# Kernel tuning notes

Hardware: AMD Instinct MI355X
Metric: run time of the kernel (lower is better)

Reference implementation:

```python
import jax, jax.numpy as jnp
import numpy as np

# graph/batch constants
B, N_PER, DEG, FEAT, K = 64, 1024, 16, 64, 10
N = B * N_PER            # 65536 total nodes
E = N * DEG              # 1048576 edges
HID = 2 * FEAT           # 128


def setup_inputs() -> dict:
    key = jax.random.key(0)
    ks = jax.random.split(key, 10)
    x = jax.random.normal(ks[0], (N, FEAT), jnp.float32)
    # intra-graph edges: local indices in [0, n) offset by graph id * n
    offs = (jnp.arange(B, dtype=jnp.int32) * N_PER)[:, None]
    edge_src = (jax.random.randint(ks[1], (B, N_PER * DEG), 0, N_PER, jnp.int32) + offs).reshape(-1)
    edge_dst = (jax.random.randint(ks[2], (B, N_PER * DEG), 0, N_PER, jnp.int32) + offs).reshape(-1)
    uniforms = jax.random.uniform(ks[3], (N, 3 * K), jnp.float32, 1e-6, 1.0 - 1e-6)

    def lin(k, i, o):
        s = 1.0 / np.sqrt(i)
        return jax.random.uniform(k, (i, o), jnp.float32, -s, s)

    return {
        "x": x, "edge_src": edge_src, "edge_dst": edge_dst, "uniforms": uniforms,
        "W0": lin(ks[4], FEAT, HID), "b0": jnp.zeros((HID,), jnp.float32),
        "W1": lin(ks[5], HID, HID), "b1": jnp.zeros((HID,), jnp.float32),
        "Wf": lin(ks[6], HID, HID), "bf": jnp.zeros((HID,), jnp.float32),
        "W2": lin(ks[7], 2 * HID, HID), "b2": jnp.zeros((HID,), jnp.float32),
        "W3": lin(ks[8], HID, 1), "b3": jnp.zeros((1,), jnp.float32),
    }


def _gcn_norm(src, dst):
    # GCNConv: add self-loops, symmetric deg^{-1/2} normalization
    loop = jnp.arange(N, dtype=src.dtype)
    s = jnp.concatenate([src, loop])
    d = jnp.concatenate([dst, loop])
    deg = jnp.zeros((N,), jnp.float32).at[d].add(1.0)
    dinv = jax.lax.rsqrt(deg)  # deg >= 1 because of self-loops
    return s, d, dinv[s] * dinv[d]


def _gcn(h, W, b, s, d, norm):
    h = h @ W                                                   # [N, out]
    agg = jnp.zeros((N, W.shape[1]), h.dtype).at[d].add(h[s] * norm[:, None])
    return agg + b


def reference(x, edge_src, edge_dst, uniforms, W0, b0, W1, b1, Wf, bf, W2, b2, W3, b3):
    s, d, norm = _gcn_norm(edge_src, edge_dst)
    # conv0 + global max pool + fc1 -> per-graph global info
    h0 = jax.nn.relu(_gcn(x, W0, b0, s, d, norm))               # [N, HID]
    glob = jnp.max(h0.reshape(B, N_PER, HID), axis=1) @ Wf + bf  # [B, HID]
    # two applications of the SAME conv1 (as in the source)
    h = jax.nn.relu(_gcn(h0, W1, b1, s, d, norm))
    h = jax.nn.relu(_gcn(h, W1, b1, s, d, norm))
    # ConcatenateLayer: [local, tiled global] per node (dropout is eval identity)
    h = jnp.concatenate([h, jnp.repeat(glob, N_PER, axis=0)], axis=-1)  # [N, 2*HID]
    h = jax.nn.relu(_gcn(h, W2, b2, s, d, norm))
    logits = _gcn(h, W3, b3, s, d, norm).reshape(B, N_PER)      # [B, n]
    # SampleConcrete (eval): per-graph top-k threshold mask
    th = jax.lax.top_k(logits, K)[0][:, -1]                     # kth-largest per graph
    mask = (logits >= th[:, None]).astype(jnp.float32)
    return mask.reshape(N, 1)
```

## Files before the change

### kernel.cpp

```cpp
#include <hip/hip_runtime.h>
#include <math.h>

#define NB    64
#define NPER  1024
#define NTOT  65536
#define ETOT  1048576
#define FEAT  64
#define HID   128
#define KSEL  10
#define MAXDEG 64


typedef __attribute__((ext_vector_type(8))) short bf16x8;
typedef __attribute__((ext_vector_type(4))) float f32x4;

static __device__ __forceinline__ unsigned short f2bf(float x) {
    unsigned u = __float_as_uint(x);
    return (unsigned short)((u + 0x7FFFu + ((u >> 16) & 1u)) >> 16);
}
static __device__ __forceinline__ float bf2f(unsigned short s) {
    return __uint_as_float(((unsigned)s) << 16);
}

__global__ __launch_bounds__(256) void csr_k(const int* __restrict__ src,
                                             const int* __restrict__ dst,
                                             int* __restrict__ cnt,
                                             unsigned short* __restrict__ col16) {
    int e = blockIdx.x * 256 + threadIdx.x;
    if (e >= ETOT) return;
    int d = dst[e];
    int s = src[e];
    int pos = atomicAdd(&cnt[d], 1);
    col16[(size_t)pos * NTOT + d] = (unsigned short)(s & (NPER - 1));
}

__global__ __launch_bounds__(256) void pack_k(const float* __restrict__ W0,
                                              const float* __restrict__ W1,
                                              const float* __restrict__ W2,
                                              unsigned short* __restrict__ Wph,
                                              unsigned short* __restrict__ Wpl,
                                              float* __restrict__ part,
                                              int* __restrict__ cnt) {
    int t = blockIdx.x * 256 + threadIdx.x;
    for (int i = t; i < NTOT; i += 160 * 256) cnt[i] = 0;
    if (blockIdx.x == 0) {
        for (int i = threadIdx.x; i < NB * 128; i += 256) part[i] = 0.f;
    }
    if (t >= 320 * 128) return;
    int k = t >> 7;
    int c = t & 127;
    float v;
    size_t mb;
    int kk;
    if (k < 64)       { kk = k;       v = W0[kk * 128 + c]; mb = 0; }
    else if (k < 192) { kk = k - 64;  v = W1[kk * 128 + c]; mb = (size_t)64 * 128; }
    else              { kk = k - 192; v = W2[kk * 128 + c]; mb = (size_t)192 * 128; }
    unsigned short h  = f2bf(v);
    unsigned short lo = f2bf(v - bf2f(h));
    size_t d = mb + ((size_t)(kk >> 3) * 128 + c) * 8 + (kk & 7);
    Wph[d] = h;
    Wpl[d] = lo;
}

__global__ __launch_bounds__(1024) void agg_k(const float* __restrict__ Z,
                                              const float* __restrict__ x,
                                              const unsigned short* __restrict__ col16,
                                              const int* __restrict__ cnt,
                                              unsigned short* __restrict__ Ah,
                                              unsigned short* __restrict__ Al,
                                              int cshift,
                                              float* __restrict__ fvec,
                                              const float* __restrict__ Wf,
                                              const float* __restrict__ bfv,
                                              const float* __restrict__ W2g,
                                              float* __restrict__ gproj,
                                              const float* __restrict__ part) {
    __shared__ float4 sy4[4096];
    int t = threadIdx.x;

    if (Wf && (int)blockIdx.x >= (int)gridDim.x - NB) {
        float* sm = (float*)sy4;
        float* mp = sm;
        float* ps = sm + 128;
        float* gl = sm + 128 + 1024;
        int gg = blockIdx.x - (gridDim.x - NB);
        int o = t & 127, s8 = t >> 7;
        if (t < 128) mp[t] = part[(size_t)gg * 128 + t];
        __syncthreads();
        float p = 0.f;
#pragma unroll
        for (int q = 0; q < 16; ++q) { int k = s8 * 16 + q; p += mp[k] * Wf[(size_t)k * 128 + o]; }
        ps[t] = p;
        __syncthreads();
        if (t < 128) {
            float a = bfv[t];
#pragma unroll
            for (int q = 0; q < 8; ++q) a += ps[q * 128 + t];
            gl[t] = a;
        }
        __syncthreads();
        p = 0.f;
#pragma unroll
        for (int q = 0; q < 16; ++q) { int k = s8 * 16 + q; p += gl[k] * W2g[(size_t)(128 + k) * 128 + o]; }
        ps[t] = p;
        __syncthreads();
        if (t < 128) {
            float a = 0.f;
#pragma unroll
            for (int q = 0; q < 8; ++q) a += ps[q * 128 + t];
            gproj[(size_t)gg * 128 + t] = a;
        }
        return;
    }

    int g = blockIdx.x >> cshift;
    int c = blockIdx.x & ((1 << cshift) - 1);
    int gbase = g << 10;

    if (x) {
#pragma unroll
        for (int j = 0; j < 4; ++j) {
            int fl = j * 1024 + t;
            int v = fl >> 2, q = fl & 3;
            float dvv = rsqrtf((float)cnt[gbase + v] + 1.0f);
            float4 z = *(const float4*)&x[(size_t)(gbase + v) * FEAT + c * 16 + q * 4];
            z.x *= dvv; z.y *= dvv; z.z *= dvv; z.w *= dvv;
            sy4[fl] = z;
        }
    } else {
        const float4* Zg4 = (const float4*)(Z + ((size_t)c * NTOT + gbase) * 16);
#pragma unroll
        for (int j = 0; j < 4; ++j) sy4[j * 1024 + t] = Zg4[j * 1024 + t];
    }
    __syncthreads();

    int f4 = t & 3;
    int vl = t >> 2;

#pragma unroll 1
    for (int pass = 0; pass < 4; ++pass) {
        int v = pass * 256 + vl;
        int gv = gbase + v;
        int n = cnt[gv];
        float dv = rsqrtf((float)n + 1.0f);
        const unsigned short* ip = col16 + gv;
        float4 acc = sy4[v * 4 + f4];
        int i = 0;
        for (; i + 4 <= n; i += 4) {
            int a0 = ip[(size_t)(i + 0) * NTOT];
            int a1 = ip[(size_t)(i + 1) * NTOT];
            int a2 = ip[(size_t)(i + 2) * NTOT];
            int a3 = ip[(size_t)(i + 3) * NTOT];
            float4 y0 = sy4[a0 * 4 + f4];
            float4 y1 = sy4[a1 * 4 + f4];
            float4 y2 = sy4[a2 * 4 + f4];
            float4 y3 = sy4[a3 * 4 + f4];
            acc.x += (y0.x + y1.x) + (y2.x + y3.x);
            acc.y += (y0.y + y1.y) + (y2.y + y3.y);
            acc.z += (y0.z + y1.z) + (y2.z + y3.z);
            acc.w += (y0.w + y1.w) + (y2.w + y3.w);
        }
        for (; i < n; ++i) {
            float4 ya = sy4[(int)ip[(size_t)i * NTOT] * 4 + f4];
            acc.x += ya.x; acc.y += ya.y; acc.z += ya.z; acc.w += ya.w;
        }
        acc.x *= dv; acc.y *= dv; acc.z *= dv; acc.w *= dv;
        int krow = c * 16 + f4 * 4;
        size_t ba = ((size_t)(krow >> 3) * NTOT + gv) * 8 + (krow & 7);
        ushort4 h, lo;
        h.x = f2bf(acc.x); lo.x = f2bf(acc.x - bf2f(h.x));
        h.y = f2bf(acc.y); lo.y = f2bf(acc.y - bf2f(h.y));
        h.z = f2bf(acc.z); lo.z = f2bf(acc.z - bf2f(h.z));
        h.w = f2bf(acc.w); lo.w = f2bf(acc.w - bf2f(h.w));
        *(ushort4*)&Ah[ba] = h;
        *(ushort4*)&Al[ba] = lo;
    }

    if (fvec && c == 0) {
        __syncthreads();
        float* sdv = (float*)sy4;
        float dv = rsqrtf((float)cnt[gbase + t] + 1.0f);
        sdv[t] = dv;
        __syncthreads();
        int n = cnt[gbase + t];
        float acc = dv;
        const unsigned short* ip = col16 + gbase + t;
        for (int i = 0; i < n; ++i) acc += sdv[ip[(size_t)i * NTOT]];
        fvec[gbase + t] = dv * acc;
    }
}

__global__ __launch_bounds__(256, 4) void gemm_k(const unsigned short* __restrict__ Ah,
                                                 const unsigned short* __restrict__ Al,
                                                 const unsigned short* __restrict__ Wph,
                                                 const unsigned short* __restrict__ Wpl,
                                                 const float* __restrict__ bias,
                                                 float* __restrict__ outZ,
                                                 int K,
                                                 const float* __restrict__ fvec,
                                                 const float* __restrict__ gproj,
                                                 float* __restrict__ part,
                                                 const float* __restrict__ W3,
                                                 const int* __restrict__ cnt,
                                                 float* __restrict__ zout) {
    __shared__ __align__(16) unsigned short sAh[64 * 128];
    __shared__ __align__(16) unsigned short sAl[64 * 128];
    __shared__ float zred[4 * 64];

    int t = threadIdx.x;
    int row0 = blockIdx.x * 64;
    int w = t >> 6;
    int l = t & 63;
    int lr = l & 15;
    int hg = l >> 4;

    f32x4 acc[4][2];
#pragma unroll
    for (int m = 0; m < 4; ++m)
#pragma unroll
        for (int n = 0; n < 2; ++n) acc[m][n] = (f32x4){0.f, 0.f, 0.f, 0.f};

    int nu = (K >> 3) << 6 >> 8;
    for (int i = 0; i < nu; ++i) {
        int u = t + i * 256;
        int p = u >> 6, r = u & 63;
        size_t src = ((size_t)p * NTOT + row0 + r) * 8;
        *(uint4*)&sAh[u * 8] = *(const uint4*)&Ah[src];
        *(uint4*)&sAl[u * 8] = *(const uint4*)&Al[src];
    }
    __syncthreads();

    int nk = K >> 5;
#pragma unroll 1
    for (int s = 0; s < nk; ++s) {
        int pb = s * 4 + hg;
        bf16x8 ah[4], al[4], bh[2], bl[2];
#pragma unroll
        for (int m = 0; m < 4; ++m) {
            ah[m] = *(const bf16x8*)&sAh[(pb * 64 + m * 16 + lr) * 8];
            al[m] = *(const bf16x8*)&sAl[(pb * 64 + m * 16 + lr) * 8];
        }
#pragma unroll
        for (int n = 0; n < 2; ++n) {
            size_t wb = ((size_t)pb * 128 + w * 32 + n * 16 + lr) * 8;
            bh[n] = *(const bf16x8*)&Wph[wb];
            bl[n] = *(const bf16x8*)&Wpl[wb];
        }
#pragma unroll
        for (int m = 0; m < 4; ++m)
#pragma unroll
            for (int n = 0; n < 2; ++n) {
                acc[m][n] = __builtin_amdgcn_mfma_f32_16x16x32_bf16(ah[m], bh[n], acc[m][n], 0, 0, 0);
                acc[m][n] = __builtin_amdgcn_mfma_f32_16x16x32_bf16(al[m], bh[n], acc[m][n], 0, 0, 0);
                acc[m][n] = __builtin_amdgcn_mfma_f32_16x16x32_bf16(ah[m], bl[n], acc[m][n], 0, 0, 0);
            }
    }

    int g = row0 >> 10;
    int wc0 = w * 32;
    float bb[2], gp[2], w3c[2];
#pragma unroll
    for (int n = 0; n < 2; ++n) {
        int col = wc0 + n * 16 + lr;
        bb[n]  = bias[col];
        gp[n]  = fvec ? gproj[(size_t)g * 128 + col] : 0.f;
        w3c[n] = zout ? W3[col] : 0.f;
    }
    float fr[4][4];
    if (fvec) {
#pragma unroll
        for (int m = 0; m < 4; ++m)
#pragma unroll
            for (int r = 0; r < 4; ++r) fr[m][r] = fvec[row0 + m * 16 + hg * 4 + r];
    }
    float dvs[4][4];
    if (outZ) {
#pragma unroll
        for (int m = 0; m < 4; ++m)
#pragma unroll
            for (int r = 0; r < 4; ++r)
                dvs[m][r] = rsqrtf((float)cnt[row0 + m * 16 + hg * 4 + r] + 1.0f);
    }
    float zp[4][4];
#pragma unroll
    for (int m = 0; m < 4; ++m)
#pragma unroll
        for (int r = 0; r < 4; ++r) zp[m][r] = 0.f;
    float cmx[2] = {0.f, 0.f};

#pragma unroll
    for (int m = 0; m < 4; ++m)
#pragma unroll
        for (int n = 0; n < 2; ++n)
#pragma unroll
            for (int r = 0; r < 4; ++r) {
                float v = acc[m][n][r] + bb[n];
                if (fvec) v += fr[m][r] * gp[n];
                v = fmaxf(v, 0.f);
                if (part) cmx[n] = fmaxf(cmx[n], v);
                if (zout) zp[m][r] += v * w3c[n];
                if (outZ) {
                    int row = row0 + m * 16 + hg * 4 + r;
                    int cidx = w * 2 + n;
                    outZ[((size_t)cidx * NTOT + row) * 16 + lr] = v * dvs[m][r];
                }
            }

    if (part) {
#pragma unroll
        for (int n = 0; n < 2; ++n) {
            float v = cmx[n];
            v = fmaxf(v, __shfl_xor(v, 16));
            v = fmaxf(v, __shfl_xor(v, 32));
            if (hg == 0)
                atomicMax((int*)&part[(size_t)g * 128 + wc0 + n * 16 + lr],
                          __float_as_int(v));
        }
    }

    if (zout) {
#pragma unroll
        for (int m = 0; m < 4; ++m)
#pragma unroll
            for (int r = 0; r < 4; ++r) {
                float v = zp[m][r];
                v += __shfl_xor(v, 1);
                v += __shfl_xor(v, 2);
                v += __shfl_xor(v, 4);
                v += __shfl_xor(v, 8);
                zp[m][r] = v;
            }
        if (lr == 0) {
#pragma unroll
            for (int m = 0; m < 4; ++m)
#pragma unroll
                for (int r = 0; r < 4; ++r)
                    zred[w * 64 + m * 16 + hg * 4 + r] = zp[m][r];
        }
        __syncthreads();
        if (t < 64) {
            float sZ = zred[t] + zred[64 + t] + zred[128 + t] + zred[192 + t];
            zout[row0 + t] = sZ * rsqrtf((float)cnt[row0 + t] + 1.0f);
        }
    }
}

__global__ __launch_bounds__(1024) void smask_k(const float* __restrict__ z,
                                                const unsigned short* __restrict__ col16,
                                                const int* __restrict__ cnt,
                                                const float* __restrict__ b3,
                                                float* __restrict__ out) {
    __shared__ float sz[1024];
    __shared__ float sl[1024];
    __shared__ float slo[1024];
    __shared__ float rv[16];
    __shared__ int   ri[16];
    __shared__ float sth;
    int g = blockIdx.x, t = threadIdx.x;
    int wv = t >> 6, ln = t & 63;
    int base = g << 10;
    sz[t] = z[base + t];
    __syncthreads();
    float bb = b3[0];
    {
        int gv = base + t;
        int n = cnt[gv];
        float dv = rsqrtf((float)n + 1.0f);
        float acc = sz[t];
        const unsigned short* ip = col16 + gv;
        int j = 0;
        for (; j + 2 <= n; j += 2)
            acc += sz[ip[(size_t)j * NTOT]] + sz[ip[(size_t)(j + 1) * NTOT]];
        for (; j < n; ++j) acc += sz[ip[(size_t)j * NTOT]];
        float lg = acc * dv + bb;
        sl[t] = lg; slo[t] = lg;
    }
    __syncthreads();
    for (int pass = 0; pass < KSEL; ++pass) {
        float bv = sl[t];
        int bi = t;
#pragma unroll
        for (int off = 32; off; off >>= 1) {
            float ov = __shfl_xor(bv, off);
            int   oi = __shfl_xor(bi, off);
            if (ov > bv || (ov == bv && oi < bi)) { bv = ov; bi = oi; }
        }
        if (ln == 0) { rv[wv] = bv; ri[wv] = bi; }
        __syncthreads();
        if (t == 0) {
            float mv = rv[0]; int mi = ri[0];
#pragma unroll
            for (int q = 1; q < 16; ++q)
                if (rv[q] > mv || (rv[q] == mv && ri[q] < mi)) { mv = rv[q]; mi = ri[q]; }
            sth = mv; sl[mi] = -INFINITY;
        }
        __syncthreads();
    }
    float th = sth;
    out[base + t] = (slo[t] >= th) ? 1.f : 0.f;
}

extern "C" void kernel_launch(void* const* d_in, const int* in_sizes, int n_in,
                              void* d_out, int out_size, void* d_ws, size_t ws_size,
                              hipStream_t stream) {
    const float* x        = (const float*)d_in[0];
    const int*   edge_src = (const int*)d_in[1];
    const int*   edge_dst = (const int*)d_in[2];
    const float* W0 = (const float*)d_in[4];
    const float* b0 = (const float*)d_in[5];
    const float* W1 = (const float*)d_in[6];
    const float* b1 = (const float*)d_in[7];
    const float* Wf = (const float*)d_in[8];
    const float* bf = (const float*)d_in[9];
    const float* W2 = (const float*)d_in[10];
    const float* b2 = (const float*)d_in[11];
    const float* W3 = (const float*)d_in[12];
    const float* b3 = (const float*)d_in[13];
    float* out = (float*)d_out;

    char* w = (char*)d_ws;
    int*            cnt   = (int*)w;            w += (size_t)NTOT * 4;
    unsigned short* col16 = (unsigned short*)w; w += (size_t)NTOT * MAXDEG * 2;
    float*          fvec  = (float*)w;          w += (size_t)NTOT * 4;
    unsigned short* Ah    = (unsigned short*)w; w += (size_t)NTOT * 128 * 2;
    unsigned short* Al    = (unsigned short*)w; w += (size_t)NTOT * 128 * 2;
    float*          Q     = (float*)w;          w += (size_t)NTOT * 128 * 4;
    float*          part  = (float*)w;          w += (size_t)NB * 128 * 4;
    float*          gproj = (float*)w;          w += (size_t)NB * 128 * 4;
    float*          z     = (float*)w;          w += (size_t)NTOT * 4;
    unsigned short* Wph   = (unsigned short*)w; w += (size_t)320 * 128 * 2;
    unsigned short* Wpl   = (unsigned short*)w; w += (size_t)320 * 128 * 2;

    pack_k<<<160, 256, 0, stream>>>(W0, W1, W2, Wph, Wpl, part, cnt);
    csr_k<<<ETOT / 256, 256, 0, stream>>>(edge_src, edge_dst, cnt, col16);

    agg_k<<<NB * 4, 1024, 0, stream>>>(nullptr, x, col16, cnt, Ah, Al, 2, nullptr,
                                       nullptr, nullptr, nullptr, nullptr, nullptr);
    gemm_k<<<NTOT / 64, 256, 0, stream>>>(Ah, Al, Wph, Wpl, b0, Q, FEAT,
                                          nullptr, nullptr, part, nullptr, cnt, nullptr);

    agg_k<<<NB * 8 + NB, 1024, 0, stream>>>(Q, nullptr, col16, cnt, Ah, Al, 3, nullptr,
                                            Wf, bf, W2, gproj, part);
    gemm_k<<<NTOT / 64, 256, 0, stream>>>(Ah, Al, Wph + 64 * 128, Wpl + 64 * 128, b1, Q,
                                          HID, nullptr, nullptr, nullptr, nullptr, cnt,
                                          nullptr);
    agg_k<<<NB * 8, 1024, 0, stream>>>(Q, nullptr, col16, cnt, Ah, Al, 3, nullptr,
                                       nullptr, nullptr, nullptr, nullptr, nullptr);
    gemm_k<<<NTOT / 64, 256, 0, stream>>>(Ah, Al, Wph + 64 * 128, Wpl + 64 * 128, b1, Q,
                                          HID, nullptr, nullptr, nullptr, nullptr, cnt,
                                          nullptr);

    agg_k<<<NB * 8, 1024, 0, stream>>>(Q, nullptr, col16, cnt, Ah, Al, 3, fvec,
                                       nullptr, nullptr, nullptr, nullptr, nullptr);
    gemm_k<<<NTOT / 64, 256, 0, stream>>>(Ah, Al, Wph + 192 * 128, Wpl + 192 * 128, b2,
                                          nullptr, HID, fvec, gproj, nullptr, W3, cnt, z);

    smask_k<<<NB, 1024, 0, stream>>>(z, col16, cnt, b3, out);
}
```

Measured before the change: 308.9 us.

## Fuse CSR build and weight packing into one kernel with shared-memory degree counters

Replaces the separate weight-packing and CSR-building kernels with one launch. One block per graph counts incoming edges with shared-memory atomics and writes the local neighbor lists, and extra blocks pack the weights and zero the partial buffer. This removes a kernel launch, the global counter zeroing pass, and global atomic contention. In exchange each graph's edges are handled by a single block, which limits parallelism to 64 blocks for the edge pass, and the code now relies on edges being grouped by graph in contiguous ranges.

```diff
diff --git a/kernel.cpp b/kernel.cpp
--- a/kernel.cpp
+++ b/kernel.cpp
@@ -22,44 +22,59 @@
     return __uint_as_float(((unsigned)s) << 16);
 }
 
-__global__ __launch_bounds__(256) void csr_k(const int* __restrict__ src,
-                                             const int* __restrict__ dst,
-                                             int* __restrict__ cnt,
-                                             unsigned short* __restrict__ col16) {
-    int e = blockIdx.x * 256 + threadIdx.x;
-    if (e >= ETOT) return;
-    int d = dst[e];
-    int s = src[e];
-    int pos = atomicAdd(&cnt[d], 1);
-    col16[(size_t)pos * NTOT + d] = (unsigned short)(s & (NPER - 1));
-}
-
-__global__ __launch_bounds__(256) void pack_k(const float* __restrict__ W0,
-                                              const float* __restrict__ W1,
-                                              const float* __restrict__ W2,
-                                              unsigned short* __restrict__ Wph,
-                                              unsigned short* __restrict__ Wpl,
-                                              float* __restrict__ part,
-                                              int* __restrict__ cnt) {
-    int t = blockIdx.x * 256 + threadIdx.x;
-    for (int i = t; i < NTOT; i += 160 * 256) cnt[i] = 0;
-    if (blockIdx.x == 0) {
-        for (int i = threadIdx.x; i < NB * 128; i += 256) part[i] = 0.f;
-    }
-    if (t >= 320 * 128) return;
-    int k = t >> 7;
-    int c = t & 127;
-    float v;
-    size_t mb;
-    int kk;
-    if (k < 64)       { kk = k;       v = W0[kk * 128 + c]; mb = 0; }
-    else if (k < 192) { kk = k - 64;  v = W1[kk * 128 + c]; mb = (size_t)64 * 128; }
-    else              { kk = k - 192; v = W2[kk * 128 + c]; mb = (size_t)192 * 128; }
-    unsigned short h  = f2bf(v);
-    unsigned short lo = f2bf(v - bf2f(h));
-    size_t d = mb + ((size_t)(kk >> 3) * 128 + c) * 8 + (kk & 7);
-    Wph[d] = h;
-    Wpl[d] = lo;
+__global__ __launch_bounds__(1024) void csrpack_k(const int* __restrict__ src,
+                                                  const int* __restrict__ dst,
+                                                  int* __restrict__ cnt,
+                                                  unsigned short* __restrict__ col16,
+                                                  const float* __restrict__ W0,
+                                                  const float* __restrict__ W1,
+                                                  const float* __restrict__ W2,
+                                                  unsigned short* __restrict__ Wph,
+                                                  unsigned short* __restrict__ Wpl,
+                                                  float* __restrict__ part) {
+    int t = threadIdx.x;
+    int b = blockIdx.x;
+    if (b >= NB) {
+        int pb = b - NB;
+        if (pb == 40) {
+            for (int i = t; i < NB * 128; i += 1024) part[i] = 0.f;
+            return;
+        }
+        int idx = pb * 1024 + t;
+        if (idx >= 320 * 128) return;
+        int k = idx >> 7;
+        int c = idx & 127;
+        float v;
+        size_t mb;
+        int kk;
+        if (k < 64)       { kk = k;       v = W0[kk * 128 + c]; mb = 0; }
+        else if (k < 192) { kk = k - 64;  v = W1[kk * 128 + c]; mb = (size_t)64 * 128; }
+        else              { kk = k - 192; v = W2[kk * 128 + c]; mb = (size_t)192 * 128; }
+        unsigned short h  = f2bf(v);
+        unsigned short lo = f2bf(v - bf2f(h));
+        size_t d = mb + ((size_t)(kk >> 3) * 128 + c) * 8 + (kk & 7);
+        Wph[d] = h;
+        Wpl[d] = lo;
+        return;
+    }
+    __shared__ int lcnt[NPER];
+    int g = b;
+    int gbase = g << 10;
+    int ebase = g * (NPER * 16);
+    lcnt[t] = 0;
+    __syncthreads();
+    const int* ds = dst + ebase;
+    const int* ss = src + ebase;
+#pragma unroll 1
+    for (int i = 0; i < 16; ++i) {
+        int e = i * 1024 + t;
+        int d = ds[e] & (NPER - 1);
+        int s = ss[e] & (NPER - 1);
+        int pos = atomicAdd(&lcnt[d], 1);
+        col16[(size_t)pos * NTOT + gbase + d] = (unsigned short)s;
+    }
+    __syncthreads();
+    cnt[gbase + t] = lcnt[t];
 }
 
 __global__ __launch_bounds__(1024) void agg_k(const float* __restrict__ Z,
@@ -431,8 +446,8 @@
     unsigned short* Wph   = (unsigned short*)w; w += (size_t)320 * 128 * 2;
     unsigned short* Wpl   = (unsigned short*)w; w += (size_t)320 * 128 * 2;
 
-    pack_k<<<160, 256, 0, stream>>>(W0, W1, W2, Wph, Wpl, part, cnt);
-    csr_k<<<ETOT / 256, 256, 0, stream>>>(edge_src, edge_dst, cnt, col16);
+    csrpack_k<<<NB + 41, 1024, 0, stream>>>(edge_src, edge_dst, cnt, col16,
+                                            W0, W1, W2, Wph, Wpl, part);
 
     agg_k<<<NB * 4, 1024, 0, stream>>>(nullptr, x, col16, cnt, Ah, Al, 2, nullptr,
                                        nullptr, nullptr, nullptr, nullptr, nullptr);
```

Measured after the change: 289.6 us. 1.07x faster.
